# Kernel optimization log

Hardware: AMD Instinct MI355X
Metric: run time of the kernel (lower is better)

Reference implementation:

```python
import jax, jax.numpy as jnp
import numpy as np

D_MODEL = 256
NUM_HEADS = 8
WINDOW = 7
B, H, W = 2, 56, 56


def setup_inputs() -> dict:
    key = jax.random.key(0)
    ks = jax.random.split(key, 9)
    s = D_MODEL ** -0.5
    return {
        "x": jax.random.normal(ks[0], (B, D_MODEL, H, W), jnp.float32),
        "wq": jax.random.normal(ks[1], (D_MODEL, D_MODEL), jnp.float32) * s,
        "bq": jnp.zeros((D_MODEL,), jnp.float32),
        "wk": jax.random.normal(ks[2], (D_MODEL, D_MODEL), jnp.float32) * s,
        "bk": jnp.zeros((D_MODEL,), jnp.float32),
        "wv": jax.random.normal(ks[3], (D_MODEL, D_MODEL), jnp.float32) * s,
        "bv": jnp.zeros((D_MODEL,), jnp.float32),
        "wo": jax.random.normal(ks[4], (D_MODEL, D_MODEL), jnp.float32) * s,
        "bo": jnp.zeros((D_MODEL,), jnp.float32),
    }


def _proj(x, w, b):
    # 1x1 conv == channel matmul. x: [B,C,H,W], w: [Cout,Cin], b: [Cout]
    return jnp.einsum('oc,bchw->bohw', w, x) + b[None, :, None, None]


def _windows(t, ws):
    # t: [B,h,d,H,W] -> [B,h,d,H,W,ws*ws], zero-padded sliding windows.
    # Row-major (i*ws + j) flattening matches torch unfold(3).unfold(4).view(...,-1).
    pad = ws // 2
    Hh, Ww = t.shape[-2], t.shape[-1]
    tp = jnp.pad(t, ((0, 0), (0, 0), (0, 0), (pad, pad), (pad, pad)))
    return jnp.stack([tp[..., i:i + Hh, j:j + Ww]
                      for i in range(ws) for j in range(ws)], axis=-1)


def reference(x, wq, bq, wk, bk, wv, bv, wo, bo):
    Bt, C, Hh, Ww = x.shape
    hd = C // NUM_HEADS
    scale = hd ** -0.5
    q = _proj(x, wq, bq).reshape(Bt, NUM_HEADS, hd, Hh, Ww)
    k = _proj(x, wk, bk).reshape(Bt, NUM_HEADS, hd, Hh, Ww)
    v = _proj(x, wv, bv).reshape(Bt, NUM_HEADS, hd, Hh, Ww)
    kw = _windows(k, WINDOW)  # [B,h,d,H,W,ws^2]
    vw = _windows(v, WINDOW)
    attn = jnp.einsum('bhdxy,bhdxyw->bhxyw', q, kw) * scale
    attn = jax.nn.softmax(attn, axis=-1)
    out = jnp.einsum('bhxyw,bhdxyw->bhdxy', attn, vw).reshape(Bt, C, Hh, Ww)
    return _proj(out, wo, bo)
```

## Files before the change

### kernel.cpp

```cpp
#include <hip/hip_runtime.h>
#include <hip/hip_bf16.h>
#include <cstdint>

#define NHEAD 8
#define HD 32
#define DM 256
#define HH 56
#define WWID 56
#define HW 3136
#define NB 2
#define SCALE 0.17677669529663687f

typedef unsigned int u32;
typedef __attribute__((ext_vector_type(8))) short short8;
typedef __attribute__((ext_vector_type(4))) float floatx4;

#define BF2F_LO(u) __uint_as_float((u) << 16)
#define BF2F_HI(u) __uint_as_float((u) & 0xffff0000u)

__global__ __launch_bounds__(256) void convert_w(
    const float* __restrict__ wq, const float* __restrict__ wk,
    const float* __restrict__ wv, const float* __restrict__ wo,
    __hip_bfloat16* __restrict__ wcat, __hip_bfloat16* __restrict__ wob)
{
    const int gid = blockIdx.x * 256 + threadIdx.x;
    const int idx4 = gid << 2;
    const int sel = idx4 >> 16;
    const int off = idx4 & 65535;
    const float* src = sel == 0 ? wq : (sel == 1 ? wk : (sel == 2 ? wv : wo));
    __hip_bfloat16* dst = sel < 3 ? (wcat + (sel << 16) + off) : (wob + off);
    float4 f = *(const float4*)&src[off];
    union { ushort4 u; __hip_bfloat16 s[4]; } pk;
    pk.s[0] = __float2bfloat16(f.x); pk.s[1] = __float2bfloat16(f.y);
    pk.s[2] = __float2bfloat16(f.z); pk.s[3] = __float2bfloat16(f.w);
    *(ushort4*)dst = pk.u;
}

__global__ __launch_bounds__(256) void transpose_x(
    const float* __restrict__ x, __hip_bfloat16* __restrict__ xT)
{
    __shared__ float tile[32][33];
    const int b = blockIdx.z, p0 = blockIdx.x * 32, c0 = blockIdx.y * 32;
    const int tx = threadIdx.x & 31, ty = threadIdx.x >> 5;
    const float* xb = x + (size_t)b * DM * HW;
    #pragma unroll
    for (int i = 0; i < 4; ++i)
        tile[ty + i * 8][tx] = xb[(size_t)(c0 + ty + i * 8) * HW + p0 + tx];
    __syncthreads();
    __hip_bfloat16* xo = xT + (size_t)b * HW * DM;
    #pragma unroll
    for (int i = 0; i < 4; ++i)
        xo[(size_t)(p0 + ty + i * 8) * DM + c0 + tx] =
            __float2bfloat16(tile[tx][ty + i * 8]);
}

template<int MODE>
__global__ __launch_bounds__(256) void gemm_mfma(
    const __hip_bfloat16* __restrict__ A,
    const __hip_bfloat16* __restrict__ Bm,
    const float* __restrict__ b0, const float* __restrict__ b1,
    const float* __restrict__ b2,
    void* __restrict__ o0, void* __restrict__ o1, void* __restrict__ o2)
{
    const int bb = blockIdx.z;
    const int n0 = blockIdx.x * 64;
    const int m0 = blockIdx.y * 128;
    const __hip_bfloat16* Bb = Bm + (size_t)bb * HW * DM + (size_t)n0 * DM;

    __shared__ __align__(16) __hip_bfloat16 As[128][40];
    __shared__ __align__(16) __hip_bfloat16 Bs[64][40];

    const int t = threadIdx.x;
    const int wave = t >> 6, lane = t & 63;
    const int quad = lane >> 4, l16 = lane & 15;
    const int mw = (wave & 1) * 64, nw = (wave >> 1) * 32;

    floatx4 acc[4][2] = {};

    const int am = t >> 2, ak = (t & 3) << 3;
    const int bn = t >> 2, bk = (t & 3) << 3;

    for (int k0g = 0; k0g < DM; k0g += 32) {
        *(uint4*)&As[am][ak]      = *(const uint4*)&A[(size_t)(m0 + am) * DM + k0g + ak];
        *(uint4*)&As[am + 64][ak] = *(const uint4*)&A[(size_t)(m0 + am + 64) * DM + k0g + ak];
        *(uint4*)&Bs[bn][bk]      = *(const uint4*)&Bb[(size_t)bn * DM + k0g + bk];
        __syncthreads();
        short8 af[4], bf[2];
        #pragma unroll
        for (int mt = 0; mt < 4; ++mt)
            af[mt] = *(const short8*)&As[mw + mt * 16 + l16][quad * 8];
        #pragma unroll
        for (int nt = 0; nt < 2; ++nt)
            bf[nt] = *(const short8*)&Bs[nw + nt * 16 + l16][quad * 8];
        #pragma unroll
        for (int mt = 0; mt < 4; ++mt)
            #pragma unroll
            for (int nt = 0; nt < 2; ++nt)
                acc[mt][nt] = __builtin_amdgcn_mfma_f32_16x16x32_bf16(
                    af[mt], bf[nt], acc[mt][nt], 0, 0, 0);
        __syncthreads();
    }

    if (MODE == 0) {
        #pragma unroll
        for (int mt = 0; mt < 4; ++mt) {
            const int gm = m0 + mw + mt * 16 + quad * 4;
            const int proj = gm >> 8;
            const int c = gm & 255;
            const int h = c >> 5, d0 = c & 31;
            const float* bptr = proj == 0 ? b0 : (proj == 1 ? b1 : b2);
            __hip_bfloat16* op = (__hip_bfloat16*)(proj == 0 ? o0 : (proj == 1 ? o1 : o2));
            const size_t base = ((size_t)(bb * NHEAD + h) * HW) * HD + d0;
            float bias[4] = {bptr[c], bptr[c + 1], bptr[c + 2], bptr[c + 3]};
            #pragma unroll
            for (int nt = 0; nt < 2; ++nt) {
                const int p = n0 + nw + nt * 16 + l16;
                union { ushort4 u; __hip_bfloat16 s[4]; } pk;
                #pragma unroll
                for (int r = 0; r < 4; ++r)
                    pk.s[r] = __float2bfloat16(acc[mt][nt][r] + bias[r]);
                *(ushort4*)&op[base + (size_t)p * HD] = pk.u;
            }
        }
    } else {
        float* yo = (float*)o0;
        #pragma unroll
        for (int mt = 0; mt < 4; ++mt) {
            const int gc = m0 + mw + mt * 16 + quad * 4;
            #pragma unroll
            for (int r = 0; r < 4; ++r) {
                const float bias = b0[gc + r];
                #pragma unroll
                for (int nt = 0; nt < 2; ++nt) {
                    const int p = n0 + nw + nt * 16 + l16;
                    yo[(size_t)(bb * DM + gc + r) * HW + p] = acc[mt][nt][r] + bias;
                }
            }
        }
    }
}

#define HROWS 8
#define HPOS  (HROWS * WWID)
#define HPP   (HPOS + 6)

__global__ __launch_bounds__(448) void attn_win(
    const __hip_bfloat16* __restrict__ q,
    const __hip_bfloat16* __restrict__ k,
    const __hip_bfloat16* __restrict__ v,
    __hip_bfloat16* __restrict__ out)
{
    __shared__ uint4 kh[HPP * 4];
    __shared__ uint4 vh[HPP * 4];

    const int t = threadIdx.x;
    const int tile = blockIdx.x;
    const int h = blockIdx.y, b = blockIdx.z;
    const int y0 = tile * 2;
    const size_t base = (size_t)(b * NHEAD + h) * HW * HD;
    const __hip_bfloat16* kp = k + base;
    const __hip_bfloat16* vp = v + base;

    #pragma unroll
    for (int it = 0; it < 4; ++it) {
        const int u = t + it * 448;
        const int pos = u >> 2, ch = u & 3;
        const int hr = pos / WWID;
        const int gx = pos - hr * WWID;
        const int gy = y0 - 3 + hr;
        uint4 kv = make_uint4(0, 0, 0, 0), vv = make_uint4(0, 0, 0, 0);
        if ((unsigned)gy < HH) {
            const size_t g = (size_t)(gy * WWID + gx) * HD + (ch << 3);
            kv = *(const uint4*)&kp[g];
            vv = *(const uint4*)&vp[g];
        }
        kh[u + 12] = kv;
        vh[u + 12] = vv;
    }
    if (t < 48) {
        const int ps = t % 6;
        const int fi = (ps < 3 ? ps * 4 : (HPOS + ps) * 4) + ((t / 6) & 3);
        const uint4 z = make_uint4(0, 0, 0, 0);
        if (t < 24) kh[fi] = z; else vh[fi] = z;
    }
    __syncthreads();

    const int pl = t >> 2;
    const int ch = t & 3;
    const int lx = pl >= WWID ? pl - WWID : pl;
    const int p = y0 * WWID + pl;

    float qf[8];
    {
        uint4 u = *(const uint4*)(q + base + (size_t)p * HD + (ch << 3));
        qf[0] = BF2F_LO(u.x); qf[1] = BF2F_HI(u.x);
        qf[2] = BF2F_LO(u.y); qf[3] = BF2F_HI(u.y);
        qf[4] = BF2F_LO(u.z); qf[5] = BF2F_HI(u.z);
        qf[6] = BF2F_LO(u.w); qf[7] = BF2F_HI(u.w);
    }

    const uint4* kb4 = kh + t;
    const uint4* vb4 = vh + t;

    float of[8] = {};
    float sum = 0.f;
    for (int i = 0; i < 7; ++i) {
        #pragma unroll
        for (int j = 0; j < 7; ++j) {
            const int off4 = (i * WWID + j) << 2;
            uint4 c0 = kb4[off4];
            float s;
            s = BF2F_LO(c0.x) * qf[0];
            s = fmaf(BF2F_HI(c0.x), qf[1], s);
            s = fmaf(BF2F_LO(c0.y), qf[2], s);
            s = fmaf(BF2F_HI(c0.y), qf[3], s);
            s = fmaf(BF2F_LO(c0.z), qf[4], s);
            s = fmaf(BF2F_HI(c0.z), qf[5], s);
            s = fmaf(BF2F_LO(c0.w), qf[6], s);
            s = fmaf(BF2F_HI(c0.w), qf[7], s);
            s += __shfl_xor(s, 1);
            s += __shfl_xor(s, 2);
            const bool xv = (unsigned)(lx + j - 3) < WWID;
            const float e = __expf(s * SCALE);
            sum += xv ? e : 1.0f;
            const float wt = xv ? e : 0.0f;
            uint4 d0 = vb4[off4];
            of[0] = fmaf(BF2F_LO(d0.x), wt, of[0]);
            of[1] = fmaf(BF2F_HI(d0.x), wt, of[1]);
            of[2] = fmaf(BF2F_LO(d0.y), wt, of[2]);
            of[3] = fmaf(BF2F_HI(d0.y), wt, of[3]);
            of[4] = fmaf(BF2F_LO(d0.z), wt, of[4]);
            of[5] = fmaf(BF2F_HI(d0.z), wt, of[5]);
            of[6] = fmaf(BF2F_LO(d0.w), wt, of[6]);
            of[7] = fmaf(BF2F_HI(d0.w), wt, of[7]);
        }
    }

    const float inv = 1.0f / sum;
    __hip_bfloat16* op = out + ((size_t)b * HW + p) * DM + h * HD + (ch << 3);
    union { uint4 u; __hip_bfloat16 s[8]; } pk;
    #pragma unroll
    for (int j = 0; j < 8; ++j)
        pk.s[j] = __float2bfloat16(of[j] * inv);
    *(uint4*)op = pk.u;
}

extern "C" void kernel_launch(void* const* d_in, const int* in_sizes, int n_in,
                              void* d_out, int out_size, void* d_ws, size_t ws_size,
                              hipStream_t stream) {
    const float* x  = (const float*)d_in[0];
    const float* wq = (const float*)d_in[1];
    const float* bq = (const float*)d_in[2];
    const float* wk = (const float*)d_in[3];
    const float* bk = (const float*)d_in[4];
    const float* wv = (const float*)d_in[5];
    const float* bv = (const float*)d_in[6];
    const float* wo = (const float*)d_in[7];
    const float* bo = (const float*)d_in[8];
    float* out = (float*)d_out;

    const size_t NPC = (size_t)NB * HW * DM;
    __hip_bfloat16* xT   = (__hip_bfloat16*)d_ws;
    __hip_bfloat16* wcat = xT + NPC;
    __hip_bfloat16* wob  = wcat + 768 * 256;
    __hip_bfloat16* qb   = wob + 256 * 256;
    __hip_bfloat16* kb   = qb + NPC;
    __hip_bfloat16* vb   = kb + NPC;
    __hip_bfloat16* attnT = vb + NPC;

    convert_w<<<256, 256, 0, stream>>>(wq, wk, wv, wo, wcat, wob);
    transpose_x<<<dim3(HW / 32, DM / 32, NB), 256, 0, stream>>>(x, xT);
    gemm_mfma<0><<<dim3(HW / 64, 6, NB), 256, 0, stream>>>(
        wcat, xT, bq, bk, bv, qb, kb, vb);
    attn_win<<<dim3(28, NHEAD, NB), 448, 0, stream>>>(qb, kb, vb, attnT);
    gemm_mfma<1><<<dim3(HW / 64, 2, NB), 256, 0, stream>>>(
        wob, attnT, bo, bo, bo, out, out, out);
}
```

Before: 116.9 us.

## Switch intermediates to fp16 with dot2 scores, fold scale into Q, merge prep kernels

Converts all intermediate storage and MFMA GEMMs from bf16 to fp16. This lets the attention kernel compute Q·K with packed fdot2 instructions instead of per-element unpack-and-FMA. The softmax scale is folded into the Q projection epilogue, and the weight conversion and x transpose kernels are merged into a single launch. fp16 has narrower range than bf16, so large activations could overflow, and the fdot2 accumulation may differ slightly in rounding.

```diff
diff --git a/kernel.cpp b/kernel.cpp
--- a/kernel.cpp
+++ b/kernel.cpp
@@ -11,53 +11,56 @@
 #define NB 2
 #define SCALE 0.17677669529663687f
 
-typedef unsigned int u32;
-typedef __attribute__((ext_vector_type(8))) short short8;
+typedef _Float16 f16;
+typedef __attribute__((ext_vector_type(2))) _Float16 f16x2;
+typedef __attribute__((ext_vector_type(8))) _Float16 f16x8;
 typedef __attribute__((ext_vector_type(4))) float floatx4;
 
-#define BF2F_LO(u) __uint_as_float((u) << 16)
-#define BF2F_HI(u) __uint_as_float((u) & 0xffff0000u)
-
-__global__ __launch_bounds__(256) void convert_w(
+union U16 { uint4 u; f16x2 h2[4]; f16 h[8]; };
+
+__global__ __launch_bounds__(256) void prep(
+    const float* __restrict__ x,
     const float* __restrict__ wq, const float* __restrict__ wk,
     const float* __restrict__ wv, const float* __restrict__ wo,
-    __hip_bfloat16* __restrict__ wcat, __hip_bfloat16* __restrict__ wob)
+    f16* __restrict__ xT, f16* __restrict__ wcat, f16* __restrict__ wob)
 {
-    const int gid = blockIdx.x * 256 + threadIdx.x;
-    const int idx4 = gid << 2;
-    const int sel = idx4 >> 16;
-    const int off = idx4 & 65535;
-    const float* src = sel == 0 ? wq : (sel == 1 ? wk : (sel == 2 ? wv : wo));
-    __hip_bfloat16* dst = sel < 3 ? (wcat + (sel << 16) + off) : (wob + off);
-    float4 f = *(const float4*)&src[off];
-    union { ushort4 u; __hip_bfloat16 s[4]; } pk;
-    pk.s[0] = __float2bfloat16(f.x); pk.s[1] = __float2bfloat16(f.y);
-    pk.s[2] = __float2bfloat16(f.z); pk.s[3] = __float2bfloat16(f.w);
-    *(ushort4*)dst = pk.u;
-}
-
-__global__ __launch_bounds__(256) void transpose_x(
-    const float* __restrict__ x, __hip_bfloat16* __restrict__ xT)
-{
-    __shared__ float tile[32][33];
-    const int b = blockIdx.z, p0 = blockIdx.x * 32, c0 = blockIdx.y * 32;
-    const int tx = threadIdx.x & 31, ty = threadIdx.x >> 5;
-    const float* xb = x + (size_t)b * DM * HW;
-    #pragma unroll
-    for (int i = 0; i < 4; ++i)
-        tile[ty + i * 8][tx] = xb[(size_t)(c0 + ty + i * 8) * HW + p0 + tx];
-    __syncthreads();
-    __hip_bfloat16* xo = xT + (size_t)b * HW * DM;
-    #pragma unroll
-    for (int i = 0; i < 4; ++i)
-        xo[(size_t)(p0 + ty + i * 8) * DM + c0 + tx] =
-            __float2bfloat16(tile[tx][ty + i * 8]);
+    const int bid = blockIdx.x;
+    const int t = threadIdx.x;
+    if (bid < 1568) {
+        __shared__ float tile[32][33];
+        const int b = bid / 784, r = bid - 784 * b;
+        const int ct = r / 98;
+        const int p0 = (r - ct * 98) * 32, c0 = ct * 32;
+        const int tx = t & 31, ty = t >> 5;
+        const float* xb = x + (size_t)b * DM * HW;
+        #pragma unroll
+        for (int i = 0; i < 4; ++i)
+            tile[ty + i * 8][tx] = xb[(size_t)(c0 + ty + i * 8) * HW + p0 + tx];
+        __syncthreads();
+        f16* xo = xT + (size_t)b * HW * DM;
+        #pragma unroll
+        for (int i = 0; i < 4; ++i)
+            xo[(size_t)(p0 + ty + i * 8) * DM + c0 + tx] =
+                (f16)tile[tx][ty + i * 8];
+    } else {
+        const int gid = (bid - 1568) * 256 + t;
+        const int idx4 = gid << 2;
+        const int sel = idx4 >> 16;
+        const int off = idx4 & 65535;
+        const float* src = sel == 0 ? wq : (sel == 1 ? wk : (sel == 2 ? wv : wo));
+        f16* dst = sel < 3 ? (wcat + (sel << 16) + off) : (wob + off);
+        float4 f = *(const float4*)&src[off];
+        union { ushort4 u; f16 h[4]; } pk;
+        pk.h[0] = (f16)f.x; pk.h[1] = (f16)f.y;
+        pk.h[2] = (f16)f.z; pk.h[3] = (f16)f.w;
+        *(ushort4*)dst = pk.u;
+    }
 }
 
 template<int MODE>
 __global__ __launch_bounds__(256) void gemm_mfma(
-    const __hip_bfloat16* __restrict__ A,
-    const __hip_bfloat16* __restrict__ Bm,
+    const f16* __restrict__ A,
+    const f16* __restrict__ Bm,
     const float* __restrict__ b0, const float* __restrict__ b1,
     const float* __restrict__ b2,
     void* __restrict__ o0, void* __restrict__ o1, void* __restrict__ o2)
@@ -65,10 +68,10 @@
     const int bb = blockIdx.z;
     const int n0 = blockIdx.x * 64;
     const int m0 = blockIdx.y * 128;
-    const __hip_bfloat16* Bb = Bm + (size_t)bb * HW * DM + (size_t)n0 * DM;
-
-    __shared__ __align__(16) __hip_bfloat16 As[128][40];
-    __shared__ __align__(16) __hip_bfloat16 Bs[64][40];
+    const f16* Bb = Bm + (size_t)bb * HW * DM + (size_t)n0 * DM;
+
+    __shared__ __align__(16) f16 As[128][40];
+    __shared__ __align__(16) f16 Bs[64][40];
 
     const int t = threadIdx.x;
     const int wave = t >> 6, lane = t & 63;
@@ -85,18 +88,18 @@
         *(uint4*)&As[am + 64][ak] = *(const uint4*)&A[(size_t)(m0 + am + 64) * DM + k0g + ak];
         *(uint4*)&Bs[bn][bk]      = *(const uint4*)&Bb[(size_t)bn * DM + k0g + bk];
         __syncthreads();
-        short8 af[4], bf[2];
+        f16x8 af[4], bf[2];
         #pragma unroll
         for (int mt = 0; mt < 4; ++mt)
-            af[mt] = *(const short8*)&As[mw + mt * 16 + l16][quad * 8];
+            af[mt] = *(const f16x8*)&As[mw + mt * 16 + l16][quad * 8];
         #pragma unroll
         for (int nt = 0; nt < 2; ++nt)
-            bf[nt] = *(const short8*)&Bs[nw + nt * 16 + l16][quad * 8];
+            bf[nt] = *(const f16x8*)&Bs[nw + nt * 16 + l16][quad * 8];
         #pragma unroll
         for (int mt = 0; mt < 4; ++mt)
             #pragma unroll
             for (int nt = 0; nt < 2; ++nt)
-                acc[mt][nt] = __builtin_amdgcn_mfma_f32_16x16x32_bf16(
+                acc[mt][nt] = __builtin_amdgcn_mfma_f32_16x16x32_f16(
                     af[mt], bf[nt], acc[mt][nt], 0, 0, 0);
         __syncthreads();
     }
@@ -109,16 +112,17 @@
             const int c = gm & 255;
             const int h = c >> 5, d0 = c & 31;
             const float* bptr = proj == 0 ? b0 : (proj == 1 ? b1 : b2);
-            __hip_bfloat16* op = (__hip_bfloat16*)(proj == 0 ? o0 : (proj == 1 ? o1 : o2));
+            f16* op = (f16*)(proj == 0 ? o0 : (proj == 1 ? o1 : o2));
+            const float sc = proj == 0 ? SCALE : 1.0f;
             const size_t base = ((size_t)(bb * NHEAD + h) * HW) * HD + d0;
             float bias[4] = {bptr[c], bptr[c + 1], bptr[c + 2], bptr[c + 3]};
             #pragma unroll
             for (int nt = 0; nt < 2; ++nt) {
                 const int p = n0 + nw + nt * 16 + l16;
-                union { ushort4 u; __hip_bfloat16 s[4]; } pk;
+                union { ushort4 u; f16 h[4]; } pk;
                 #pragma unroll
                 for (int r = 0; r < 4; ++r)
-                    pk.s[r] = __float2bfloat16(acc[mt][nt][r] + bias[r]);
+                    pk.h[r] = (f16)((acc[mt][nt][r] + bias[r]) * sc);
                 *(ushort4*)&op[base + (size_t)p * HD] = pk.u;
             }
         }
@@ -145,10 +149,10 @@
 #define HPP   (HPOS + 6)
 
 __global__ __launch_bounds__(448) void attn_win(
-    const __hip_bfloat16* __restrict__ q,
-    const __hip_bfloat16* __restrict__ k,
-    const __hip_bfloat16* __restrict__ v,
-    __hip_bfloat16* __restrict__ out)
+    const f16* __restrict__ q,
+    const f16* __restrict__ k,
+    const f16* __restrict__ v,
+    f16* __restrict__ out)
 {
     __shared__ uint4 kh[HPP * 4];
     __shared__ uint4 vh[HPP * 4];
@@ -158,8 +162,8 @@
     const int h = blockIdx.y, b = blockIdx.z;
     const int y0 = tile * 2;
     const size_t base = (size_t)(b * NHEAD + h) * HW * HD;
-    const __hip_bfloat16* kp = k + base;
-    const __hip_bfloat16* vp = v + base;
+    const f16* kp = k + base;
+    const f16* vp = v + base;
 
     #pragma unroll
     for (int it = 0; it < 4; ++it) {
@@ -190,14 +194,8 @@
     const int lx = pl >= WWID ? pl - WWID : pl;
     const int p = y0 * WWID + pl;
 
-    float qf[8];
-    {
-        uint4 u = *(const uint4*)(q + base + (size_t)p * HD + (ch << 3));
-        qf[0] = BF2F_LO(u.x); qf[1] = BF2F_HI(u.x);
-        qf[2] = BF2F_LO(u.y); qf[3] = BF2F_HI(u.y);
-        qf[4] = BF2F_LO(u.z); qf[5] = BF2F_HI(u.z);
-        qf[6] = BF2F_LO(u.w); qf[7] = BF2F_HI(u.w);
-    }
+    U16 qu;
+    qu.u = *(const uint4*)(q + base + (size_t)p * HD + (ch << 3));
 
     const uint4* kb4 = kh + t;
     const uint4* vb4 = vh + t;
@@ -208,41 +206,37 @@
         #pragma unroll
         for (int j = 0; j < 7; ++j) {
             const int off4 = (i * WWID + j) << 2;
-            uint4 c0 = kb4[off4];
+            U16 ku; ku.u = kb4[off4];
             float s;
-            s = BF2F_LO(c0.x) * qf[0];
-            s = fmaf(BF2F_HI(c0.x), qf[1], s);
-            s = fmaf(BF2F_LO(c0.y), qf[2], s);
-            s = fmaf(BF2F_HI(c0.y), qf[3], s);
-            s = fmaf(BF2F_LO(c0.z), qf[4], s);
-            s = fmaf(BF2F_HI(c0.z), qf[5], s);
-            s = fmaf(BF2F_LO(c0.w), qf[6], s);
-            s = fmaf(BF2F_HI(c0.w), qf[7], s);
+            s = __builtin_amdgcn_fdot2(ku.h2[0], qu.h2[0], 0.0f, false);
+            s = __builtin_amdgcn_fdot2(ku.h2[1], qu.h2[1], s, false);
+            s = __builtin_amdgcn_fdot2(ku.h2[2], qu.h2[2], s, false);
+            s = __builtin_amdgcn_fdot2(ku.h2[3], qu.h2[3], s, false);
             s += __shfl_xor(s, 1);
             s += __shfl_xor(s, 2);
             const bool xv = (unsigned)(lx + j - 3) < WWID;
-            const float e = __expf(s * SCALE);
+            const float e = __expf(s);
             sum += xv ? e : 1.0f;
             const float wt = xv ? e : 0.0f;
-            uint4 d0 = vb4[off4];
-            of[0] = fmaf(BF2F_LO(d0.x), wt, of[0]);
-            of[1] = fmaf(BF2F_HI(d0.x), wt, of[1]);
-            of[2] = fmaf(BF2F_LO(d0.y), wt, of[2]);
-            of[3] = fmaf(BF2F_HI(d0.y), wt, of[3]);
-            of[4] = fmaf(BF2F_LO(d0.z), wt, of[4]);
-            of[5] = fmaf(BF2F_HI(d0.z), wt, of[5]);
-            of[6] = fmaf(BF2F_LO(d0.w), wt, of[6]);
-            of[7] = fmaf(BF2F_HI(d0.w), wt, of[7]);
+            U16 vu; vu.u = vb4[off4];
+            of[0] = fmaf((float)vu.h[0], wt, of[0]);
+            of[1] = fmaf((float)vu.h[1], wt, of[1]);
+            of[2] = fmaf((float)vu.h[2], wt, of[2]);
+            of[3] = fmaf((float)vu.h[3], wt, of[3]);
+            of[4] = fmaf((float)vu.h[4], wt, of[4]);
+            of[5] = fmaf((float)vu.h[5], wt, of[5]);
+            of[6] = fmaf((float)vu.h[6], wt, of[6]);
+            of[7] = fmaf((float)vu.h[7], wt, of[7]);
         }
     }
 
     const float inv = 1.0f / sum;
-    __hip_bfloat16* op = out + ((size_t)b * HW + p) * DM + h * HD + (ch << 3);
-    union { uint4 u; __hip_bfloat16 s[8]; } pk;
+    f16* op = out + ((size_t)b * HW + p) * DM + h * HD + (ch << 3);
+    U16 ou;
     #pragma unroll
     for (int j = 0; j < 8; ++j)
-        pk.s[j] = __float2bfloat16(of[j] * inv);
-    *(uint4*)op = pk.u;
+        ou.h[j] = (f16)(of[j] * inv);
+    *(uint4*)op = ou.u;
 }
 
 extern "C" void kernel_launch(void* const* d_in, const int* in_sizes, int n_in,
@@ -260,16 +254,15 @@
     float* out = (float*)d_out;
 
     const size_t NPC = (size_t)NB * HW * DM;
-    __hip_bfloat16* xT   = (__hip_bfloat16*)d_ws;
-    __hip_bfloat16* wcat = xT + NPC;
-    __hip_bfloat16* wob  = wcat + 768 * 256;
-    __hip_bfloat16* qb   = wob + 256 * 256;
-    __hip_bfloat16* kb   = qb + NPC;
-    __hip_bfloat16* vb   = kb + NPC;
-    __hip_bfloat16* attnT = vb + NPC;
-
-    convert_w<<<256, 256, 0, stream>>>(wq, wk, wv, wo, wcat, wob);
-    transpose_x<<<dim3(HW / 32, DM / 32, NB), 256, 0, stream>>>(x, xT);
+    f16* xT    = (f16*)d_ws;
+    f16* wcat  = xT + NPC;
+    f16* wob   = wcat + 768 * 256;
+    f16* qb    = wob + 256 * 256;
+    f16* kb    = qb + NPC;
+    f16* vb    = kb + NPC;
+    f16* attnT = vb + NPC;
+
+    prep<<<1824, 256, 0, stream>>>(x, wq, wk, wv, wo, xT, wcat, wob);
     gemm_mfma<0><<<dim3(HW / 64, 6, NB), 256, 0, stream>>>(
         wcat, xT, bq, bk, bv, qb, kb, vb);
     attn_win<<<dim3(28, NHEAD, NB), 448, 0, stream>>>(qb, kb, vb, attnT);
```

Result: faster. 111.7 us (-4.5%).
